# Kernel tuning notes

Hardware: AMD Instinct MI355X
Metric: run time of the kernel (lower is better)

The kernel has to match this reference:

```python
import jax, jax.numpy as jnp
import numpy as np

TEMP = 0.05  # contrastive temperature (ContrastiveLoss.temp)
N, D = 8192, 128


def setup_inputs() -> dict:
    key = jax.random.key(0)
    k1, k2 = jax.random.split(key)
    x = jax.random.normal(k1, (N, D), dtype=jnp.float32)
    # Binary positive-pair label matrix; diagonal forced to 1 so every row
    # has at least one positive (positive_pair_nums > 0).
    y = (jax.random.uniform(k2, (N, N)) < 0.05).astype(jnp.float32)
    y = jnp.maximum(y, jnp.eye(N, dtype=jnp.float32))
    return {"x": x, "y": y}


def reference(x, y):
    # similarity(): L2-normalize rows, cosine matmul, exp(cos / temp)
    x_norm = x / jnp.linalg.norm(x, axis=1, keepdims=True)        # [N, D]
    cos_sim = jnp.exp(jnp.matmul(x_norm, x_norm.T) / TEMP)        # [N, N]

    positive_pair_nums = jnp.sum(y, axis=-1)                      # [N]
    neg_y = 1.0 - y
    # hard_mode == 'normal': negative mass per anchor
    nl = jnp.sum(cos_sim * neg_y, axis=-1, keepdims=True)         # [N, 1]

    # sm = log(cos_sim / (cos_sim + nl)); average over positives per row
    sm = jnp.log(cos_sim / (cos_sim + nl))                        # [N, N]
    lm = jnp.sum(sm * y, axis=-1) / positive_pair_nums            # [N]
    return -jnp.mean(lm)
```

## Files before the change

### kernel.cpp

```cpp
#include <hip/hip_runtime.h>
#include <hip/hip_bf16.h>


#define NN 8192

typedef short bf16x8 __attribute__((ext_vector_type(8)));
typedef float f32x4 __attribute__((ext_vector_type(4)));
typedef unsigned long long u64;
typedef unsigned int u32;

__device__ inline unsigned short f32_to_bf16_rne(float f) {
    unsigned u = __float_as_uint(f);
    unsigned r = 0x7FFFu + ((u >> 16) & 1u);
    return (unsigned short)((u + r) >> 16);
}

__global__ __launch_bounds__(256) void prep_kernel(
    const float* __restrict__ x, const float* __restrict__ y,
    unsigned short* __restrict__ xn, u64* __restrict__ bits) {
    const int t = threadIdx.x;
    const int w = t >> 6, l = t & 63;
    if (blockIdx.x < 2048) {
        const int row = blockIdx.x * 4 + w;
        float2 v = reinterpret_cast<const float2*>(x)[row * 64 + l];
        float ss = v.x * v.x + v.y * v.y;
#pragma unroll
        for (int m = 1; m < 64; m <<= 1) ss += __shfl_xor(ss, m);
        float rn = 1.0f / sqrtf(ss);
        ushort2 st;
        st.x = f32_to_bf16_rne(v.x * rn);
        st.y = f32_to_bf16_rne(v.y * rn);
        reinterpret_cast<ushort2*>(xn)[row * 64 + l] = st;
    } else {
        const int gw = (blockIdx.x - 2048) * 4 + w;
#pragma unroll 1
        for (int it = 0; it < 32; ++it) {
            const size_t w0 = ((size_t)it * 8192 + gw) * 4;
            u64 m0 = __ballot(y[(w0 + 0) * 64 + l] != 0.0f);
            u64 m1 = __ballot(y[(w0 + 1) * 64 + l] != 0.0f);
            u64 m2 = __ballot(y[(w0 + 2) * 64 + l] != 0.0f);
            u64 m3 = __ballot(y[(w0 + 3) * 64 + l] != 0.0f);
            if (l == 0) {
                bits[w0 + 0] = m0;
                bits[w0 + 1] = m1;
                bits[w0 + 2] = m2;
                bits[w0 + 3] = m3;
            }
        }
    }
}

template <bool DIAG>
__device__ __forceinline__ void epilogue(
    const f32x4 (&acc)[4][4], const u64 (&bw)[4], int l, int lm16, int lh4,
    int wM, int wN, int R0, int cb, float* __restrict__ Pt,
    float* __restrict__ sdg) {
#pragma unroll
    for (int qq = 0; qq < 4; ++qq) {
        float T = 0.0f, A = 0.0f, Y = 0.0f;
        const u32 lo = (u32)bw[qq];
        const u32 hi = (u32)(bw[qq] >> 32);
        const int rl = qq * 16 + lm16;
#pragma unroll
        for (int p = 0; p < 4; ++p) {
            const u32 wsel = (p < 2) ? lo : hi;
#pragma unroll
            for (int j = 0; j < 4; ++j) {
                float s = 20.0f * acc[p][qq][j];
                float e = __expf(s);
                float yv = (float)((wsel >> ((p & 1) * 16 + lh4 + j)) & 1u);
                if (DIAG) {
                    if (wM == wN && (p * 16 + lh4 + j) == rl) {
                        sdg[R0 + rl] = s;
                        e = 0.0f;
                        yv = 0.0f;
                    }
                }
                T += e;
                A = fmaf(yv, s, A);
                Y = fmaf(yv, e, Y);
            }
        }
        T += __shfl_xor(T, 16); T += __shfl_xor(T, 32);
        A += __shfl_xor(A, 16); A += __shfl_xor(A, 32);
        Y += __shfl_xor(Y, 16); Y += __shfl_xor(Y, 32);
        if (l < 16) {
            const size_t idx = (size_t)(cb * 2 + wM) * NN + (R0 + qq * 16 + l);
            Pt[idx] = T;
            Pt[1048576 + idx] = A;
            Pt[2 * 1048576 + idx] = Y;
        }
    }
}

__global__ __launch_bounds__(256, 3) void contrast_main_kernel(
    const unsigned short* __restrict__ xn, const u64* __restrict__ bits,
    float* __restrict__ Pt, float* __restrict__ sdg) {
    const int cb = blockIdx.x, rb = blockIdx.y;
    const int t = threadIdx.x;
    const int w = t >> 6, l = t & 63;
    const int wM = w >> 1, wN = w & 1;
    const int lm16 = l & 15, lh = l >> 4, lh4 = lh << 2;

    const int C0 = cb * 128 + wM * 64;
    const int R0 = rb * 128 + wN * 64;

    u64 bw[4];
#pragma unroll
    for (int qq = 0; qq < 4; ++qq)
        bw[qq] = bits[(size_t)(R0 + qq * 16 + lm16) * 128 + cb * 2 + wM];

    f32x4 acc[4][4];
#pragma unroll
    for (int i = 0; i < 4; ++i)
#pragma unroll
        for (int j = 0; j < 4; ++j) {
            f32x4 z = {0.0f, 0.0f, 0.0f, 0.0f};
            acc[i][j] = z;
        }

    const char* xb = reinterpret_cast<const char*>(xn);
#pragma unroll
    for (int ks = 0; ks < 4; ++ks) {
        bf16x8 af[4], bfr[4];
#pragma unroll
        for (int p = 0; p < 4; ++p) {
            const size_t c = (size_t)(C0 + p * 16 + lm16);
            af[p] = *reinterpret_cast<const bf16x8*>(xb + c * 256 + ks * 64 +
                                                     lh * 16);
        }
#pragma unroll
        for (int qq = 0; qq < 4; ++qq) {
            const size_t r = (size_t)(R0 + qq * 16 + lm16);
            bfr[qq] = *reinterpret_cast<const bf16x8*>(xb + r * 256 + ks * 64 +
                                                       lh * 16);
        }
#pragma unroll
        for (int p = 0; p < 4; ++p)
#pragma unroll
            for (int qq = 0; qq < 4; ++qq)
                acc[p][qq] = __builtin_amdgcn_mfma_f32_16x16x32_bf16(
                    af[p], bfr[qq], acc[p][qq], 0, 0, 0);
    }

    if (cb == rb)
        epilogue<true>(acc, bw, l, lm16, lh4, wM, wN, R0, cb, Pt, sdg);
    else
        epilogue<false>(acc, bw, l, lm16, lh4, wM, wN, R0, cb, Pt, sdg);
}

__global__ __launch_bounds__(256) void finalize_kernel(
    const float* __restrict__ Pt, const u64* __restrict__ bits,
    const float* __restrict__ sdg, float* __restrict__ out) {
    const int t = threadIdx.x;
    const int w = t >> 6, l = t & 63;
    const int r = blockIdx.x * 4 + w;

    const size_t base = (size_t)l * NN + r;
    float T = Pt[base] + Pt[base + (size_t)64 * NN];
    float A = Pt[1048576 + base] + Pt[1048576 + base + (size_t)64 * NN];
    float Y = Pt[2 * 1048576 + base] + Pt[2 * 1048576 + base + (size_t)64 * NN];
    u64 b0 = bits[(size_t)r * 128 + l];
    u64 b1 = bits[(size_t)r * 128 + 64 + l];
    float Pc = (float)(__popcll(b0) + __popcll(b1));
#pragma unroll
    for (int m = 1; m < 64; m <<= 1) {
        T += __shfl_xor(T, m);
        A += __shfl_xor(A, m);
        Y += __shfl_xor(Y, m);
        Pc += __shfl_xor(Pc, m);
    }

    __shared__ float red[4];
    if (l == 0) {
        const float nl = T - Y;
        const float sd = sdg[r];
        red[w] = (A - (Pc - 1.0f) * logf(nl) - log1pf(nl * __expf(-sd))) / Pc;
    }
    __syncthreads();
    if (t == 0) {
        float s = red[0] + red[1] + red[2] + red[3];
        atomicAdd(out, -s * (1.0f / (float)NN));
    }
}

extern "C" void kernel_launch(void* const* d_in, const int* in_sizes, int n_in,
                              void* d_out, int out_size, void* d_ws,
                              size_t ws_size, hipStream_t stream) {
    const float* x = (const float*)d_in[0];
    const float* y = (const float*)d_in[1];

    char* ws = (char*)d_ws;
    unsigned short* xn = (unsigned short*)ws;
    u64* bits = (u64*)(ws + (2ull << 20));
    float* Pt = (float*)(ws + (10ull << 20));
    float* sdg = (float*)(ws + (22ull << 20));

    hipMemsetAsync(d_out, 0, sizeof(float), stream);
    prep_kernel<<<4096, 256, 0, stream>>>(x, y, xn, bits);
    contrast_main_kernel<<<dim3(64, 64), 256, 0, stream>>>(xn, bits, Pt, sdg);
    finalize_kernel<<<NN / 4, 256, 0, stream>>>(Pt, bits, sdg, (float*)d_out);
}
```

Measured before the change: 473.6 us.

## Fuse label reading into GEMM kernel with LDS double-buffered column panels

Drops the separate pass that packed the label matrix into bitmasks. The main kernel now reads the float labels directly, prefetching the next tile's labels into registers alongside the GEMM. Each block keeps its row panel resident in LDS, loaded via global_load_lds with an XOR swizzle, and double-buffers 16 column panels, overlapping loads with MFMA work. Per-row partial sums, now including a positive count, are stored row-major for a simpler finalize. The diagonal self-similarity term is replaced by the constant exp(-20), and the GEMM-computed diagonal value is no longer saved.

```diff
diff --git a/kernel.cpp b/kernel.cpp
--- a/kernel.cpp
+++ b/kernel.cpp
@@ -6,8 +6,6 @@
 
 typedef short bf16x8 __attribute__((ext_vector_type(8)));
 typedef float f32x4 __attribute__((ext_vector_type(4)));
-typedef unsigned long long u64;
-typedef unsigned int u32;
 
 __device__ inline unsigned short f32_to_bf16_rne(float f) {
     unsigned u = __float_as_uint(f);
@@ -15,63 +13,42 @@
     return (unsigned short)((u + r) >> 16);
 }
 
-__global__ __launch_bounds__(256) void prep_kernel(
-    const float* __restrict__ x, const float* __restrict__ y,
-    unsigned short* __restrict__ xn, u64* __restrict__ bits) {
+__global__ __launch_bounds__(256) void norm_kernel(
+    const float* __restrict__ x, unsigned short* __restrict__ xn) {
     const int t = threadIdx.x;
     const int w = t >> 6, l = t & 63;
-    if (blockIdx.x < 2048) {
-        const int row = blockIdx.x * 4 + w;
-        float2 v = reinterpret_cast<const float2*>(x)[row * 64 + l];
-        float ss = v.x * v.x + v.y * v.y;
-#pragma unroll
-        for (int m = 1; m < 64; m <<= 1) ss += __shfl_xor(ss, m);
-        float rn = 1.0f / sqrtf(ss);
-        ushort2 st;
-        st.x = f32_to_bf16_rne(v.x * rn);
-        st.y = f32_to_bf16_rne(v.y * rn);
-        reinterpret_cast<ushort2*>(xn)[row * 64 + l] = st;
-    } else {
-        const int gw = (blockIdx.x - 2048) * 4 + w;
-#pragma unroll 1
-        for (int it = 0; it < 32; ++it) {
-            const size_t w0 = ((size_t)it * 8192 + gw) * 4;
-            u64 m0 = __ballot(y[(w0 + 0) * 64 + l] != 0.0f);
-            u64 m1 = __ballot(y[(w0 + 1) * 64 + l] != 0.0f);
-            u64 m2 = __ballot(y[(w0 + 2) * 64 + l] != 0.0f);
-            u64 m3 = __ballot(y[(w0 + 3) * 64 + l] != 0.0f);
-            if (l == 0) {
-                bits[w0 + 0] = m0;
-                bits[w0 + 1] = m1;
-                bits[w0 + 2] = m2;
-                bits[w0 + 3] = m3;
-            }
-        }
-    }
+    const int row = blockIdx.x * 4 + w;
+    float2 v = reinterpret_cast<const float2*>(x)[row * 64 + l];
+    float ss = v.x * v.x + v.y * v.y;
+#pragma unroll
+    for (int m = 1; m < 64; m <<= 1) ss += __shfl_xor(ss, m);
+    float rn = 1.0f / sqrtf(ss);
+    ushort2 st;
+    st.x = f32_to_bf16_rne(v.x * rn);
+    st.y = f32_to_bf16_rne(v.y * rn);
+    reinterpret_cast<ushort2*>(xn)[row * 64 + l] = st;
 }
 
 template <bool DIAG>
 __device__ __forceinline__ void epilogue(
-    const f32x4 (&acc)[4][4], const u64 (&bw)[4], int l, int lm16, int lh4,
-    int wM, int wN, int R0, int cb, float* __restrict__ Pt,
-    float* __restrict__ sdg) {
-#pragma unroll
-    for (int qq = 0; qq < 4; ++qq) {
-        float T = 0.0f, A = 0.0f, Y = 0.0f;
-        const u32 lo = (u32)bw[qq];
-        const u32 hi = (u32)(bw[qq] >> 32);
-        const int rl = qq * 16 + lm16;
+    const f32x4 (&acc)[4][2], const f32x4 (&yv4)[2][4], int wM, int wN,
+    int lm16, int lh, int l, int rb, int cb, float* __restrict__ PtT,
+    float* __restrict__ PtA, float* __restrict__ PtY,
+    float* __restrict__ PtP) {
+#pragma unroll
+    for (int qq = 0; qq < 2; ++qq) {
+        float T = 0.0f, A = 0.0f, Y = 0.0f, Pc = 0.0f;
+        const int rl = wN * 32 + qq * 16 + lm16;
 #pragma unroll
         for (int p = 0; p < 4; ++p) {
-            const u32 wsel = (p < 2) ? lo : hi;
+            const int cl = wM * 64 + p * 16 + lh * 4;
 #pragma unroll
             for (int j = 0; j < 4; ++j) {
                 float s = 20.0f * acc[p][qq][j];
                 float e = __expf(s);
-                float yv = (float)((wsel >> ((p & 1) * 16 + lh4 + j)) & 1u);
+                float yv = (yv4[qq][p][j] != 0.0f) ? 1.0f : 0.0f;
                 if (DIAG) {
-                    if (wM == wN && (p * 16 + lh4 + j) == rl) {
-                        sdg[R0 + rl] = s;
+                    if (cl + j == rl) {
                         e = 0.0f;
                         yv = 0.0f;
                     }
@@ -79,90 +56,163 @@
                 T += e;
                 A = fmaf(yv, s, A);
                 Y = fmaf(yv, e, Y);
+                Pc += yv;
             }
         }
         T += __shfl_xor(T, 16); T += __shfl_xor(T, 32);
         A += __shfl_xor(A, 16); A += __shfl_xor(A, 32);
         Y += __shfl_xor(Y, 16); Y += __shfl_xor(Y, 32);
+        Pc += __shfl_xor(Pc, 16); Pc += __shfl_xor(Pc, 32);
         if (l < 16) {
-            const size_t idx = (size_t)(cb * 2 + wM) * NN + (R0 + qq * 16 + l);
-            Pt[idx] = T;
-            Pt[1048576 + idx] = A;
-            Pt[2 * 1048576 + idx] = Y;
-        }
-    }
-}
-
-__global__ __launch_bounds__(256, 3) void contrast_main_kernel(
-    const unsigned short* __restrict__ xn, const u64* __restrict__ bits,
-    float* __restrict__ Pt, float* __restrict__ sdg) {
-    const int cb = blockIdx.x, rb = blockIdx.y;
+            const size_t o =
+                (size_t)(rb * 128 + wN * 32 + qq * 16 + l) * 128 + cb * 2 + wM;
+            PtT[o] = T;
+            PtA[o] = A;
+            PtY[o] = Y;
+            PtP[o] = Pc;
+        }
+    }
+}
+
+__global__ __launch_bounds__(512, 2) void contrast_main_kernel(
+    const unsigned short* __restrict__ xn, const float* __restrict__ y,
+    float* __restrict__ PtT, float* __restrict__ PtA,
+    float* __restrict__ PtY, float* __restrict__ PtP) {
+    __shared__ __align__(1024) char lds[98304];
+
+    const int b = blockIdx.x;
+    const int rb = b >> 2;
+    const int cb0 = (b & 3) * 16;
     const int t = threadIdx.x;
     const int w = t >> 6, l = t & 63;
-    const int wM = w >> 1, wN = w & 1;
-    const int lm16 = l & 15, lh = l >> 4, lh4 = lh << 2;
-
-    const int C0 = cb * 128 + wM * 64;
-    const int R0 = rb * 128 + wN * 64;
-
-    u64 bw[4];
-#pragma unroll
-    for (int qq = 0; qq < 4; ++qq)
-        bw[qq] = bits[(size_t)(R0 + qq * 16 + lm16) * 128 + cb * 2 + wM];
-
-    f32x4 acc[4][4];
-#pragma unroll
-    for (int i = 0; i < 4; ++i)
-#pragma unroll
-        for (int j = 0; j < 4; ++j) {
-            f32x4 z = {0.0f, 0.0f, 0.0f, 0.0f};
-            acc[i][j] = z;
-        }
-
+    const int wM = w & 1, wN = w >> 1;
+    const int lm16 = l & 15, lh = l >> 4;
     const char* xb = reinterpret_cast<const char*>(xn);
-#pragma unroll
-    for (int ks = 0; ks < 4; ++ks) {
-        bf16x8 af[4], bfr[4];
-#pragma unroll
-        for (int p = 0; p < 4; ++p) {
-            const size_t c = (size_t)(C0 + p * 16 + lm16);
-            af[p] = *reinterpret_cast<const bf16x8*>(xb + c * 256 + ks * 64 +
-                                                     lh * 16);
-        }
-#pragma unroll
-        for (int qq = 0; qq < 4; ++qq) {
-            const size_t r = (size_t)(R0 + qq * 16 + lm16);
-            bfr[qq] = *reinterpret_cast<const bf16x8*>(xb + r * 256 + ks * 64 +
-                                                       lh * 16);
-        }
-#pragma unroll
-        for (int p = 0; p < 4; ++p)
-#pragma unroll
-            for (int qq = 0; qq < 4; ++qq)
-                acc[p][qq] = __builtin_amdgcn_mfma_f32_16x16x32_bf16(
-                    af[p], bfr[qq], acc[p][qq], 0, 0, 0);
-    }
-
-    if (cb == rb)
-        epilogue<true>(acc, bw, l, lm16, lh4, wM, wN, R0, cb, Pt, sdg);
-    else
-        epilogue<false>(acc, bw, l, lm16, lh4, wM, wN, R0, cb, Pt, sdg);
-}
-
-__global__ __launch_bounds__(256) void finalize_kernel(
-    const float* __restrict__ Pt, const u64* __restrict__ bits,
-    const float* __restrict__ sdg, float* __restrict__ out) {
+
+    {
+        const char* srcR = xb + (size_t)rb * 32768;
+        const char* srcC = xb + (size_t)cb0 * 32768;
+#pragma unroll
+        for (int i = 0; i < 4; ++i) {
+            const int p = i * 8192 + t * 16;
+            const int src = p ^ (((p >> 8) & 7) << 4);
+            __builtin_amdgcn_global_load_lds(
+                (const __attribute__((address_space(1))) void*)(srcR + src),
+                (__attribute__((address_space(3))) void*)(lds + p), 16, 0, 0);
+        }
+#pragma unroll
+        for (int i = 0; i < 4; ++i) {
+            const int p = i * 8192 + t * 16;
+            const int src = p ^ (((p >> 8) & 7) << 4);
+            __builtin_amdgcn_global_load_lds(
+                (const __attribute__((address_space(1))) void*)(srcC + src),
+                (__attribute__((address_space(3))) void*)(lds + 32768 + p), 16,
+                0, 0);
+        }
+    }
+    f32x4 ycA[2][4], ycB[2][4];
+    const int R0l = rb * 128 + wN * 32 + lm16;
+    {
+        const int C0 = cb0 * 128 + wM * 64 + lh * 4;
+#pragma unroll
+        for (int qq = 0; qq < 2; ++qq)
+#pragma unroll
+            for (int p = 0; p < 4; ++p)
+                ycA[qq][p] = *reinterpret_cast<const f32x4*>(
+                    y + (size_t)(R0l + qq * 16) * NN + C0 + p * 16);
+    }
+
+#pragma unroll 1
+    for (int it = 0; it < 16; ++it) {
+        const int cb = cb0 + it;
+        if (it < 15) {
+            const char* srcC = xb + (size_t)(cb + 1) * 32768;
+            char* dst = lds + 32768 + ((it + 1) & 1) * 32768;
+#pragma unroll
+            for (int i = 0; i < 4; ++i) {
+                const int p = i * 8192 + t * 16;
+                const int src = p ^ (((p >> 8) & 7) << 4);
+                __builtin_amdgcn_global_load_lds(
+                    (const __attribute__((address_space(1))) void*)(srcC + src),
+                    (__attribute__((address_space(3))) void*)(dst + p), 16, 0,
+                    0);
+            }
+            const int C0n = (cb + 1) * 128 + wM * 64 + lh * 4;
+#pragma unroll
+            for (int qq = 0; qq < 2; ++qq)
+#pragma unroll
+                for (int p = 0; p < 4; ++p)
+                    ycB[qq][p] = *reinterpret_cast<const f32x4*>(
+                        y + (size_t)(R0l + qq * 16) * NN + C0n + p * 16);
+            asm volatile("s_waitcnt vmcnt(12)" ::: "memory");
+        } else {
+            asm volatile("s_waitcnt vmcnt(0)" ::: "memory");
+        }
+        __builtin_amdgcn_s_barrier();
+
+        const char* cpan = lds + 32768 + (it & 1) * 32768;
+        f32x4 acc[4][2];
+#pragma unroll
+        for (int i = 0; i < 4; ++i)
+#pragma unroll
+            for (int j = 0; j < 2; ++j) {
+                f32x4 z = {0.0f, 0.0f, 0.0f, 0.0f};
+                acc[i][j] = z;
+            }
+#pragma unroll
+        for (int ks = 0; ks < 4; ++ks) {
+            bf16x8 af[4], bfr[2];
+#pragma unroll
+            for (int p = 0; p < 4; ++p) {
+                const int c = wM * 64 + p * 16 + lm16;
+                const int v = c * 256 + ks * 64 + lh * 16;
+                af[p] = *reinterpret_cast<const bf16x8*>(
+                    cpan + (v ^ ((c & 7) << 4)));
+            }
+#pragma unroll
+            for (int qq = 0; qq < 2; ++qq) {
+                const int r = wN * 32 + qq * 16 + lm16;
+                const int v = r * 256 + ks * 64 + lh * 16;
+                bfr[qq] = *reinterpret_cast<const bf16x8*>(
+                    lds + (v ^ ((r & 7) << 4)));
+            }
+#pragma unroll
+            for (int p = 0; p < 4; ++p)
+#pragma unroll
+                for (int qq = 0; qq < 2; ++qq)
+                    acc[p][qq] = __builtin_amdgcn_mfma_f32_16x16x32_bf16(
+                        af[p], bfr[qq], acc[p][qq], 0, 0, 0);
+        }
+
+        if (rb == cb)
+            epilogue<true>(acc, ycA, wM, wN, lm16, lh, l, rb, cb, PtT, PtA,
+                           PtY, PtP);
+        else
+            epilogue<false>(acc, ycA, wM, wN, lm16, lh, l, rb, cb, PtT, PtA,
+                            PtY, PtP);
+        __builtin_amdgcn_s_barrier();
+
+#pragma unroll
+        for (int qq = 0; qq < 2; ++qq)
+#pragma unroll
+            for (int p = 0; p < 4; ++p) ycA[qq][p] = ycB[qq][p];
+    }
+}
+
+__global__ __launch_bounds__(1024) void finalize_kernel(
+    const float* __restrict__ PtT, const float* __restrict__ PtA,
+    const float* __restrict__ PtY, const float* __restrict__ PtP,
+    float* __restrict__ out) {
     const int t = threadIdx.x;
     const int w = t >> 6, l = t & 63;
-    const int r = blockIdx.x * 4 + w;
-
-    const size_t base = (size_t)l * NN + r;
-    float T = Pt[base] + Pt[base + (size_t)64 * NN];
-    float A = Pt[1048576 + base] + Pt[1048576 + base + (size_t)64 * NN];
-    float Y = Pt[2 * 1048576 + base] + Pt[2 * 1048576 + base + (size_t)64 * NN];
-    u64 b0 = bits[(size_t)r * 128 + l];
-    u64 b1 = bits[(size_t)r * 128 + 64 + l];
-    float Pc = (float)(__popcll(b0) + __popcll(b1));
+    const int r = blockIdx.x * 16 + w;
+
+    float2 vT = reinterpret_cast<const float2*>(PtT + (size_t)r * 128)[l];
+    float2 vA = reinterpret_cast<const float2*>(PtA + (size_t)r * 128)[l];
+    float2 vY = reinterpret_cast<const float2*>(PtY + (size_t)r * 128)[l];
+    float2 vP = reinterpret_cast<const float2*>(PtP + (size_t)r * 128)[l];
+    float T = vT.x + vT.y, A = vA.x + vA.y, Y = vY.x + vY.y,
+          Pc = vP.x + vP.y;
 #pragma unroll
     for (int m = 1; m < 64; m <<= 1) {
         T += __shfl_xor(T, m);
@@ -170,16 +220,17 @@
         Y += __shfl_xor(Y, m);
         Pc += __shfl_xor(Pc, m);
     }
-
-    __shared__ float red[4];
+    __shared__ float red[16];
     if (l == 0) {
+        const float P = Pc + 1.0f;
         const float nl = T - Y;
-        const float sd = sdg[r];
-        red[w] = (A - (Pc - 1.0f) * logf(nl) - log1pf(nl * __expf(-sd))) / Pc;
+        red[w] = (A - (P - 1.0f) * logf(nl) - log1pf(nl * 2.0611536e-9f)) / P;
     }
     __syncthreads();
     if (t == 0) {
-        float s = red[0] + red[1] + red[2] + red[3];
+        float s = 0.0f;
+#pragma unroll
+        for (int i = 0; i < 16; ++i) s += red[i];
         atomicAdd(out, -s * (1.0f / (float)NN));
     }
 }
@@ -192,12 +243,14 @@
 
     char* ws = (char*)d_ws;
     unsigned short* xn = (unsigned short*)ws;
-    u64* bits = (u64*)(ws + (2ull << 20));
-    float* Pt = (float*)(ws + (10ull << 20));
-    float* sdg = (float*)(ws + (22ull << 20));
+    float* PtT = (float*)(ws + (2ull << 20));
+    float* PtA = (float*)(ws + (6ull << 20));
+    float* PtY = (float*)(ws + (10ull << 20));
+    float* PtP = (float*)(ws + (14ull << 20));
 
     hipMemsetAsync(d_out, 0, sizeof(float), stream);
-    prep_kernel<<<4096, 256, 0, stream>>>(x, y, xn, bits);
-    contrast_main_kernel<<<dim3(64, 64), 256, 0, stream>>>(xn, bits, Pt, sdg);
-    finalize_kernel<<<NN / 4, 256, 0, stream>>>(Pt, bits, sdg, (float*)d_out);
-}
+    norm_kernel<<<NN / 4, 256, 0, stream>>>(x, xn);
+    contrast_main_kernel<<<256, 512, 0, stream>>>(xn, y, PtT, PtA, PtY, PtP);
+    finalize_kernel<<<NN / 16, 1024, 0, stream>>>(PtT, PtA, PtY, PtP,
+                                                  (float*)d_out);
+}
```

New measurement: 418.2 us. 11.7% less time.
